# Optimization experiments

Hardware: AMD Instinct MI355X
Metric: run time of the kernel (lower is better)

## Reference

```python
import jax, jax.numpy as jnp
import numpy as np

NUM_QUBITS = 4
SHOTS = 1000
BATCH = 8192
IN_SIZE = 4096
OUT_SIZE = 4096


def setup_inputs() -> dict:
    key = jax.random.key(0)
    k_x, k_w, k_b, k_q = jax.random.split(key, 4)
    x = jax.random.normal(k_x, (BATCH, IN_SIZE), dtype=jnp.float32)
    W = jax.random.normal(k_w, (OUT_SIZE, IN_SIZE), dtype=jnp.float32) * (1.0 / np.sqrt(IN_SIZE))
    b = jax.random.normal(k_b, (OUT_SIZE,), dtype=jnp.float32) * 0.01
    # Each shot's measurement outcome: num_qubits independent uniform bits
    # == one uniform integer in [0, 2**num_qubits).
    quantum_outcomes = jax.random.randint(k_q, (BATCH, SHOTS), 0, 2 ** NUM_QUBITS, dtype=jnp.int32)
    return {"x": x, "W": W, "b": b, "quantum_outcomes": quantum_outcomes}


def reference(x, W, b, quantum_outcomes):
    # classical path: nn.Linear
    classical = jnp.einsum("bi,oi->bo", x, W) + b  # [B, OUT]
    # normalized by max outcome, broadcast across the output dim.
    max_outcome = float(2 ** NUM_QUBITS - 1)
    expectation = jnp.mean(quantum_outcomes.astype(jnp.float32), axis=1) / max_outcome  # [B]
    return classical + expectation[:, None]
```

## Files before the change

kernel.cpp:

```cpp
#include <hip/hip_runtime.h>
#include <hip/hip_bf16.h>

typedef __attribute__((ext_vector_type(8))) short short8;
typedef __attribute__((ext_vector_type(4))) float f32x4;
typedef unsigned short ushort_t;

#define BM 128
#define BN 128
#define BK 64

__device__ __forceinline__ ushort_t f2bf_rne(float f) {
    unsigned u = __float_as_uint(f);
    u += 0x7FFF + ((u >> 16) & 1);
    return (ushort_t)(u >> 16);
}

__global__ void expect_kernel(const int* __restrict__ q, float* __restrict__ e,
                              int rows, int shots) {
    int row = blockIdx.x * (blockDim.x >> 6) + (threadIdx.x >> 6);
    int lane = threadIdx.x & 63;
    if (row >= rows) return;
    const int* rp = q + (long long)row * shots;
    int s = 0;
    for (int j = lane; j < shots; j += 64) s += rp[j];
    #pragma unroll
    for (int off = 32; off; off >>= 1) s += __shfl_down(s, off, 64);
    if (lane == 0) e[row] = (float)s * (1.0f / (1000.0f * 15.0f));
}

__device__ __forceinline__ short8 pack8(float4 a, float4 b) {
    short8 r;
    r[0] = (short)f2bf_rne(a.x); r[1] = (short)f2bf_rne(a.y);
    r[2] = (short)f2bf_rne(a.z); r[3] = (short)f2bf_rne(a.w);
    r[4] = (short)f2bf_rne(b.x); r[5] = (short)f2bf_rne(b.y);
    r[6] = (short)f2bf_rne(b.z); r[7] = (short)f2bf_rne(b.w);
    return r;
}

__global__ void cvt2_kernel(const float* __restrict__ x, ushort_t* __restrict__ xb,
                            const float* __restrict__ w, ushort_t* __restrict__ wb,
                            int blocks_x) {
    const float* src; ushort_t* dst; long long base;
    if (blockIdx.x < blocks_x) {
        src = x; dst = xb; base = (long long)blockIdx.x * blockDim.x;
    } else {
        src = w; dst = wb; base = (long long)(blockIdx.x - blocks_x) * blockDim.x;
    }
    long long i = base + threadIdx.x;
    float4 a = ((const float4*)src)[2 * i];
    float4 b = ((const float4*)src)[2 * i + 1];
    ((short8*)dst)[i] = pack8(a, b);
}

__global__ __launch_bounds__(256, 2)
void gemm_kernel(const ushort_t* __restrict__ A, const ushort_t* __restrict__ B,
                 const float* __restrict__ bias, const float* __restrict__ expect,
                 float* __restrict__ C, int M, int N, int K) {
    __shared__ ushort_t As[BM * BK];
    __shared__ ushort_t Bs[BN * BK];

    const int num_pid_n = N / BN;
    const int GROUP = 8;
    int pid = blockIdx.x;
    int group_size = GROUP * num_pid_n;
    int gid = pid / group_size;
    int pin = pid - gid * group_size;
    int pid_m = gid * GROUP + (pin % GROUP);
    int pid_n = pin / GROUP;

    const int tid  = threadIdx.x;
    const int lane = tid & 63;
    const int wave = tid >> 6;
    const int wm = (wave >> 1) * 64;
    const int wn = (wave & 1) * 64;

    const int srow = tid >> 3;
    const int slot = tid & 7;
    const int gchunk = slot ^ (srow & 7);

    const ushort_t* a_ptr = A + (long long)pid_m * BM * K + gchunk * 8;
    const ushort_t* b_ptr = B + (long long)pid_n * BN * K + gchunk * 8;

    f32x4 acc[4][4];
    #pragma unroll
    for (int i = 0; i < 4; i++)
        #pragma unroll
        for (int j = 0; j < 4; j++)
            acc[i][j] = (f32x4)(0.0f);

    const int quad = lane >> 4;
    const int l15  = lane & 15;
    const int rlow = l15 & 7;

    for (int k0 = 0; k0 < K; k0 += BK) {
        #pragma unroll
        for (int s = 0; s < 4; s++) {
            int row = srow + s * 32;
            __builtin_amdgcn_global_load_lds(
                (const __attribute__((address_space(1))) unsigned int*)(a_ptr + (long long)row * K + k0),
                (__attribute__((address_space(3))) unsigned int*)(As + row * BK + slot * 8),
                16, 0, 0);
        }
        #pragma unroll
        for (int s = 0; s < 4; s++) {
            int row = srow + s * 32;
            __builtin_amdgcn_global_load_lds(
                (const __attribute__((address_space(1))) unsigned int*)(b_ptr + (long long)row * K + k0),
                (__attribute__((address_space(3))) unsigned int*)(Bs + row * BK + slot * 8),
                16, 0, 0);
        }
        __syncthreads();

        #pragma unroll
        for (int ks = 0; ks < 2; ks++) {
            int q = ks * 4 + quad;
            int sw = (q ^ rlow) * 8;
            short8 af[4], bf[4];
            #pragma unroll
            for (int i = 0; i < 4; i++) {
                af[i] = *(const short8*)(As + (wm + i * 16 + l15) * BK + sw);
                bf[i] = *(const short8*)(Bs + (wn + i * 16 + l15) * BK + sw);
            }
            #pragma unroll
            for (int i = 0; i < 4; i++)
                #pragma unroll
                for (int j = 0; j < 4; j++)
                    acc[i][j] = __builtin_amdgcn_mfma_f32_16x16x32_bf16(
                        af[i], bf[j], acc[i][j], 0, 0, 0);
        }
        __syncthreads();
    }

    long long row0 = (long long)pid_m * BM + wm;
    int col0 = pid_n * BN + wn;
    #pragma unroll
    for (int j = 0; j < 4; j++) {
        int col = col0 + j * 16 + l15;
        float bj = bias[col];
        #pragma unroll
        for (int i = 0; i < 4; i++) {
            #pragma unroll
            for (int r = 0; r < 4; r++) {
                long long row = row0 + i * 16 + quad * 4 + r;
                C[row * N + col] = acc[i][j][r] + bj + expect[row];
            }
        }
    }
}

__global__ __launch_bounds__(256, 2)
void gemm_f32stage_kernel(const float* __restrict__ A, const float* __restrict__ B,
                          const float* __restrict__ bias, const float* __restrict__ expect,
                          float* __restrict__ C, int M, int N, int K) {
    __shared__ ushort_t As[BM * BK];
    __shared__ ushort_t Bs[BN * BK];

    const int num_pid_n = N / BN;
    const int GROUP = 8;
    int pid = blockIdx.x;
    int group_size = GROUP * num_pid_n;
    int gid = pid / group_size;
    int pin = pid - gid * group_size;
    int pid_m = gid * GROUP + (pin % GROUP);
    int pid_n = pin / GROUP;

    const int tid  = threadIdx.x;
    const int lane = tid & 63;
    const int wave = tid >> 6;
    const int wm = (wave >> 1) * 64;
    const int wn = (wave & 1) * 64;

    const int srow = tid >> 1;
    const int chalf = (tid & 1) * 4;

    const float* a_base = A + ((long long)pid_m * BM + srow) * K + chalf * 8;
    const float* b_base = B + ((long long)pid_n * BN + srow) * K + chalf * 8;

    f32x4 acc[4][4];
    #pragma unroll
    for (int i = 0; i < 4; i++)
        #pragma unroll
        for (int j = 0; j < 4; j++)
            acc[i][j] = (f32x4)(0.0f);

    const int quad = lane >> 4;
    const int l15  = lane & 15;
    const int rlow = l15 & 7;

    for (int k0 = 0; k0 < K; k0 += BK) {
        {
            const float4* ap = (const float4*)(a_base + k0);
            const float4* bp = (const float4*)(b_base + k0);
            float4 fa[8], fb[8];
            #pragma unroll
            for (int c = 0; c < 8; c++) { fa[c] = ap[c]; fb[c] = bp[c]; }
            #pragma unroll
            for (int c = 0; c < 4; c++) {
                int sl = ((chalf + c) ^ (srow & 7)) * 8;
                *(short8*)(As + srow * BK + sl) = pack8(fa[2*c], fa[2*c+1]);
                *(short8*)(Bs + srow * BK + sl) = pack8(fb[2*c], fb[2*c+1]);
            }
        }
        __syncthreads();

        #pragma unroll
        for (int ks = 0; ks < 2; ks++) {
            int q = ks * 4 + quad;
            int sw = (q ^ rlow) * 8;
            short8 af[4], bf[4];
            #pragma unroll
            for (int i = 0; i < 4; i++) {
                af[i] = *(const short8*)(As + (wm + i * 16 + l15) * BK + sw);
                bf[i] = *(const short8*)(Bs + (wn + i * 16 + l15) * BK + sw);
            }
            #pragma unroll
            for (int i = 0; i < 4; i++)
                #pragma unroll
                for (int j = 0; j < 4; j++)
                    acc[i][j] = __builtin_amdgcn_mfma_f32_16x16x32_bf16(
                        af[i], bf[j], acc[i][j], 0, 0, 0);
        }
        __syncthreads();
    }

    long long row0 = (long long)pid_m * BM + wm;
    int col0 = pid_n * BN + wn;
    #pragma unroll
    for (int j = 0; j < 4; j++) {
        int col = col0 + j * 16 + l15;
        float bj = bias[col];
        #pragma unroll
        for (int i = 0; i < 4; i++) {
            #pragma unroll
            for (int r = 0; r < 4; r++) {
                long long row = row0 + i * 16 + quad * 4 + r;
                C[row * N + col] = acc[i][j][r] + bj + expect[row];
            }
        }
    }
}

extern "C" void kernel_launch(void* const* d_in, const int* in_sizes, int n_in,
                              void* d_out, int out_size, void* d_ws, size_t ws_size,
                              hipStream_t stream) {
    const float* x = (const float*)d_in[0];
    const float* W = (const float*)d_in[1];
    const float* b = (const float*)d_in[2];
    const int*   q = (const int*)d_in[3];
    float* out = (float*)d_out;

    const int M = 8192, N = 4096, K = 4096, SHOTS = 1000;

    float* expect = (float*)d_ws;
    size_t need = 32768 + (size_t)M * K * 2 + (size_t)N * K * 2;

    expect_kernel<<<M / 4, 256, 0, stream>>>(q, expect, M, SHOTS);

    if (ws_size >= need) {
        ushort_t* xb = (ushort_t*)((char*)d_ws + 32768);
        ushort_t* wb = xb + (size_t)M * K;
        int blocks_x = (int)((long long)M * K / 8 / 256);
        int blocks_w = (int)((long long)N * K / 8 / 256);
        cvt2_kernel<<<blocks_x + blocks_w, 256, 0, stream>>>(x, xb, W, wb, blocks_x);
        gemm_kernel<<<(M / BM) * (N / BN), 256, 0, stream>>>(xb, wb, b, expect, out, M, N, K);
    } else {
        gemm_f32stage_kernel<<<(M / BM) * (N / BN), 256, 0, stream>>>(x, W, b, expect, out, M, N, K);
    }
}
```

Before: 589.8 us.

## Fuse expectation reduction into conversion kernel and remap GEMM tiles per XCD

The expectation reduction is folded into the bf16 conversion kernel, removing one launch. Each conversion thread now handles 16 floats instead of 8. The GEMM tile ordering is replaced: the low 3 bits of the block id select an XCD-local group of 4 N-tiles, and M advances slowly. This aims to improve L2 reuse of W tiles within each chiplet, at the risk of worse reuse of A rows across XCDs.

Result: faster. 549.8 us (-6.8%).

```diff
diff --git a/kernel.cpp b/kernel.cpp
--- a/kernel.cpp
+++ b/kernel.cpp
@@ -13,6 +13,137 @@
     unsigned u = __float_as_uint(f);
     u += 0x7FFF + ((u >> 16) & 1);
     return (ushort_t)(u >> 16);
+}
+
+__device__ __forceinline__ short8 pack8(float4 a, float4 b) {
+    short8 r;
+    r[0] = (short)f2bf_rne(a.x); r[1] = (short)f2bf_rne(a.y);
+    r[2] = (short)f2bf_rne(a.z); r[3] = (short)f2bf_rne(a.w);
+    r[4] = (short)f2bf_rne(b.x); r[5] = (short)f2bf_rne(b.y);
+    r[6] = (short)f2bf_rne(b.z); r[7] = (short)f2bf_rne(b.w);
+    return r;
+}
+
+__global__ void prep_kernel(const float* __restrict__ x, ushort_t* __restrict__ xb,
+                            const float* __restrict__ w, ushort_t* __restrict__ wb,
+                            const int* __restrict__ q, float* __restrict__ e,
+                            int blocks_x, int blocks_w, int shots) {
+    int bid = blockIdx.x;
+    if (bid < blocks_x + blocks_w) {
+        const float* src; ushort_t* dst; long long base;
+        if (bid < blocks_x) { src = x; dst = xb; base = (long long)bid * blockDim.x; }
+        else { src = w; dst = wb; base = (long long)(bid - blocks_x) * blockDim.x; }
+        long long i = base + threadIdx.x;
+        float4 a0 = ((const float4*)src)[4 * i];
+        float4 a1 = ((const float4*)src)[4 * i + 1];
+        float4 a2 = ((const float4*)src)[4 * i + 2];
+        float4 a3 = ((const float4*)src)[4 * i + 3];
+        ((short8*)dst)[2 * i]     = pack8(a0, a1);
+        ((short8*)dst)[2 * i + 1] = pack8(a2, a3);
+    } else {
+        int eb = bid - (blocks_x + blocks_w);
+        int row = eb * 4 + (threadIdx.x >> 6);
+        int lane = threadIdx.x & 63;
+        const int* rp = q + (long long)row * shots;
+        int s = 0;
+        for (int j = lane; j < shots; j += 64) s += rp[j];
+        #pragma unroll
+        for (int off = 32; off; off >>= 1) s += __shfl_down(s, off, 64);
+        if (lane == 0) e[row] = (float)s * (1.0f / (1000.0f * 15.0f));
+    }
+}
+
+__global__ __launch_bounds__(256, 2)
+void gemm_kernel(const ushort_t* __restrict__ A, const ushort_t* __restrict__ B,
+                 const float* __restrict__ bias, const float* __restrict__ expect,
+                 float* __restrict__ C, int M, int N, int K) {
+    __shared__ ushort_t As[BM * BK];
+    __shared__ ushort_t Bs[BN * BK];
+
+    int pid = blockIdx.x;
+    const int xcd = pid & 7;
+    const int p   = pid >> 3;
+    int pid_n = xcd * 4 + (p & 3);
+    int pid_m = p >> 2;
+
+    const int tid  = threadIdx.x;
+    const int lane = tid & 63;
+    const int wave = tid >> 6;
+    const int wm = (wave >> 1) * 64;
+    const int wn = (wave & 1) * 64;
+
+    const int srow = tid >> 3;
+    const int slot = tid & 7;
+    const int gchunk = slot ^ (srow & 7);
+
+    const ushort_t* a_ptr = A + (long long)pid_m * BM * K + gchunk * 8;
+    const ushort_t* b_ptr = B + (long long)pid_n * BN * K + gchunk * 8;
+
+    f32x4 acc[4][4];
+    #pragma unroll
+    for (int i = 0; i < 4; i++)
+        #pragma unroll
+        for (int j = 0; j < 4; j++)
+            acc[i][j] = (f32x4)(0.0f);
+
+    const int quad = lane >> 4;
+    const int l15  = lane & 15;
+    const int rlow = l15 & 7;
+
+    for (int k0 = 0; k0 < K; k0 += BK) {
+        #pragma unroll
+        for (int s = 0; s < 4; s++) {
+            int row = srow + s * 32;
+            __builtin_amdgcn_global_load_lds(
+                (const __attribute__((address_space(1))) unsigned int*)(a_ptr + (long long)row * K + k0),
+                (__attribute__((address_space(3))) unsigned int*)(As + row * BK + slot * 8),
+                16, 0, 0);
+        }
+        #pragma unroll
+        for (int s = 0; s < 4; s++) {
+            int row = srow + s * 32;
+            __builtin_amdgcn_global_load_lds(
+                (const __attribute__((address_space(1))) unsigned int*)(b_ptr + (long long)row * K + k0),
+                (__attribute__((address_space(3))) unsigned int*)(Bs + row * BK + slot * 8),
+                16, 0, 0);
+        }
+        __syncthreads();
+
+        #pragma unroll
+        for (int ks = 0; ks < 2; ks++) {
+            int q = ks * 4 + quad;
+            int sw = (q ^ rlow) * 8;
+            short8 af[4], bf[4];
+            #pragma unroll
+            for (int i = 0; i < 4; i++) {
+                af[i] = *(const short8*)(As + (wm + i * 16 + l15) * BK + sw);
+                bf[i] = *(const short8*)(Bs + (wn + i * 16 + l15) * BK + sw);
+            }
+            #pragma unroll
+            for (int i = 0; i < 4; i++)
+                #pragma unroll
+                for (int j = 0; j < 4; j++)
+                    acc[i][j] = __builtin_amdgcn_mfma_f32_16x16x32_bf16(
+                        af[i], bf[j], acc[i][j], 0, 0, 0);
+        }
+        __syncthreads();
+    }
+
+    long long row0 = (long long)pid_m * BM + wm;
+    int col0 = pid_n * BN + wn;
+    #pragma unroll
+    for (int j = 0; j < 4; j++) {
+        int col = col0 + j * 16 + l15;
+        float bj = bias[col];
+        #pragma unroll
+        for (int i = 0; i < 4; i++) {
+            #pragma unroll
+            for (int r = 0; r < 4; r++) {
+                long long row = row0 + i * 16 + quad * 4 + r;
+                C[row * N + col] = acc[i][j][r] + bj + expect[row];
+            }
+        }
+    }
 }
 
 __global__ void expect_kernel(const int* __restrict__ q, float* __restrict__ e,
@@ -28,126 +159,6 @@
     if (lane == 0) e[row] = (float)s * (1.0f / (1000.0f * 15.0f));
 }
 
-__device__ __forceinline__ short8 pack8(float4 a, float4 b) {
-    short8 r;
-    r[0] = (short)f2bf_rne(a.x); r[1] = (short)f2bf_rne(a.y);
-    r[2] = (short)f2bf_rne(a.z); r[3] = (short)f2bf_rne(a.w);
-    r[4] = (short)f2bf_rne(b.x); r[5] = (short)f2bf_rne(b.y);
-    r[6] = (short)f2bf_rne(b.z); r[7] = (short)f2bf_rne(b.w);
-    return r;
-}
-
-__global__ void cvt2_kernel(const float* __restrict__ x, ushort_t* __restrict__ xb,
-                            const float* __restrict__ w, ushort_t* __restrict__ wb,
-                            int blocks_x) {
-    const float* src; ushort_t* dst; long long base;
-    if (blockIdx.x < blocks_x) {
-        src = x; dst = xb; base = (long long)blockIdx.x * blockDim.x;
-    } else {
-        src = w; dst = wb; base = (long long)(blockIdx.x - blocks_x) * blockDim.x;
-    }
-    long long i = base + threadIdx.x;
-    float4 a = ((const float4*)src)[2 * i];
-    float4 b = ((const float4*)src)[2 * i + 1];
-    ((short8*)dst)[i] = pack8(a, b);
-}
-
-__global__ __launch_bounds__(256, 2)
-void gemm_kernel(const ushort_t* __restrict__ A, const ushort_t* __restrict__ B,
-                 const float* __restrict__ bias, const float* __restrict__ expect,
-                 float* __restrict__ C, int M, int N, int K) {
-    __shared__ ushort_t As[BM * BK];
-    __shared__ ushort_t Bs[BN * BK];
-
-    const int num_pid_n = N / BN;
-    const int GROUP = 8;
-    int pid = blockIdx.x;
-    int group_size = GROUP * num_pid_n;
-    int gid = pid / group_size;
-    int pin = pid - gid * group_size;
-    int pid_m = gid * GROUP + (pin % GROUP);
-    int pid_n = pin / GROUP;
-
-    const int tid  = threadIdx.x;
-    const int lane = tid & 63;
-    const int wave = tid >> 6;
-    const int wm = (wave >> 1) * 64;
-    const int wn = (wave & 1) * 64;
-
-    const int srow = tid >> 3;
-    const int slot = tid & 7;
-    const int gchunk = slot ^ (srow & 7);
-
-    const ushort_t* a_ptr = A + (long long)pid_m * BM * K + gchunk * 8;
-    const ushort_t* b_ptr = B + (long long)pid_n * BN * K + gchunk * 8;
-
-    f32x4 acc[4][4];
-    #pragma unroll
-    for (int i = 0; i < 4; i++)
-        #pragma unroll
-        for (int j = 0; j < 4; j++)
-            acc[i][j] = (f32x4)(0.0f);
-
-    const int quad = lane >> 4;
-    const int l15  = lane & 15;
-    const int rlow = l15 & 7;
-
-    for (int k0 = 0; k0 < K; k0 += BK) {
-        #pragma unroll
-        for (int s = 0; s < 4; s++) {
-            int row = srow + s * 32;
-            __builtin_amdgcn_global_load_lds(
-                (const __attribute__((address_space(1))) unsigned int*)(a_ptr + (long long)row * K + k0),
-                (__attribute__((address_space(3))) unsigned int*)(As + row * BK + slot * 8),
-                16, 0, 0);
-        }
-        #pragma unroll
-        for (int s = 0; s < 4; s++) {
-            int row = srow + s * 32;
-            __builtin_amdgcn_global_load_lds(
-                (const __attribute__((address_space(1))) unsigned int*)(b_ptr + (long long)row * K + k0),
-                (__attribute__((address_space(3))) unsigned int*)(Bs + row * BK + slot * 8),
-                16, 0, 0);
-        }
-        __syncthreads();
-
-        #pragma unroll
-        for (int ks = 0; ks < 2; ks++) {
-            int q = ks * 4 + quad;
-            int sw = (q ^ rlow) * 8;
-            short8 af[4], bf[4];
-            #pragma unroll
-            for (int i = 0; i < 4; i++) {
-                af[i] = *(const short8*)(As + (wm + i * 16 + l15) * BK + sw);
-                bf[i] = *(const short8*)(Bs + (wn + i * 16 + l15) * BK + sw);
-            }
-            #pragma unroll
-            for (int i = 0; i < 4; i++)
-                #pragma unroll
-                for (int j = 0; j < 4; j++)
-                    acc[i][j] = __builtin_amdgcn_mfma_f32_16x16x32_bf16(
-                        af[i], bf[j], acc[i][j], 0, 0, 0);
-        }
-        __syncthreads();
-    }
-
-    long long row0 = (long long)pid_m * BM + wm;
-    int col0 = pid_n * BN + wn;
-    #pragma unroll
-    for (int j = 0; j < 4; j++) {
-        int col = col0 + j * 16 + l15;
-        float bj = bias[col];
-        #pragma unroll
-        for (int i = 0; i < 4; i++) {
-            #pragma unroll
-            for (int r = 0; r < 4; r++) {
-                long long row = row0 + i * 16 + quad * 4 + r;
-                C[row * N + col] = acc[i][j][r] + bj + expect[row];
-            }
-        }
-    }
-}
-
 __global__ __launch_bounds__(256, 2)
 void gemm_f32stage_kernel(const float* __restrict__ A, const float* __restrict__ B,
                           const float* __restrict__ bias, const float* __restrict__ expect,
@@ -155,14 +166,11 @@
     __shared__ ushort_t As[BM * BK];
     __shared__ ushort_t Bs[BN * BK];
 
-    const int num_pid_n = N / BN;
-    const int GROUP = 8;
     int pid = blockIdx.x;
-    int group_size = GROUP * num_pid_n;
-    int gid = pid / group_size;
-    int pin = pid - gid * group_size;
-    int pid_m = gid * GROUP + (pin % GROUP);
-    int pid_n = pin / GROUP;
+    const int xcd = pid & 7;
+    const int p   = pid >> 3;
+    int pid_n = xcd * 4 + (p & 3);
+    int pid_m = p >> 2;
 
     const int tid  = threadIdx.x;
     const int lane = tid & 63;
@@ -254,16 +262,17 @@
     float* expect = (float*)d_ws;
     size_t need = 32768 + (size_t)M * K * 2 + (size_t)N * K * 2;
 
-    expect_kernel<<<M / 4, 256, 0, stream>>>(q, expect, M, SHOTS);
-
     if (ws_size >= need) {
         ushort_t* xb = (ushort_t*)((char*)d_ws + 32768);
         ushort_t* wb = xb + (size_t)M * K;
-        int blocks_x = (int)((long long)M * K / 8 / 256);
-        int blocks_w = (int)((long long)N * K / 8 / 256);
-        cvt2_kernel<<<blocks_x + blocks_w, 256, 0, stream>>>(x, xb, W, wb, blocks_x);
+        int blocks_x = (int)((long long)M * K / 16 / 256);
+        int blocks_w = (int)((long long)N * K / 16 / 256);
+        int blocks_e = M / 4;
+        prep_kernel<<<blocks_x + blocks_w + blocks_e, 256, 0, stream>>>(
+            x, xb, W, wb, q, expect, blocks_x, blocks_w, SHOTS);
         gemm_kernel<<<(M / BM) * (N / BN), 256, 0, stream>>>(xb, wb, b, expect, out, M, N, K);
     } else {
+        expect_kernel<<<M / 4, 256, 0, stream>>>(q, expect, M, SHOTS);
         gemm_f32stage_kernel<<<(M / BM) * (N / BN), 256, 0, stream>>>(x, W, b, expect, out, M, N, K);
     }
 }
```
